# Kernel tuning notes

Hardware: AMD Instinct MI355X
Metric: run time of the kernel (lower is better)

## Reference

```python
import jax, jax.numpy as jnp
import numpy as np

B, N, W, H, D, HEADS, L, T, FT = 1, 8192, 32, 128, 128, 4, 3, 2048, 768
NW = N // W          # 256 query windows
DH = D // HEADS      # 32 head dim
NEG = jnp.float32(-1e9)

def _ln(x):
    m = jnp.mean(x, axis=-1, keepdims=True)
    v = jnp.var(x, axis=-1, keepdims=True)
    return (x - m) * jax.lax.rsqrt(v + 1e-5)

def setup_inputs():
    ks = iter(jax.random.split(jax.random.key(0), 40))
    f = lambda shape, s=0.02: jax.random.normal(next(ks), shape, jnp.float32) * s
    return dict(
        q=f((B, N, D), 1.0),
        c=f((B, N, D), 1.0),
        r=f((B, N, 3), 1.0),
        atom_enc_bias=f((B, NW, HEADS, W, H), 1.0),
        token_ids=jax.random.randint(next(ks), (B, N), 0, T),
        key_indices=jnp.sort(jax.random.randint(next(ks), (B, NW, H), 0, N), axis=-1),
        atom_pad_mask=jnp.ones((B, N), jnp.bool_),
        r_to_q_w=f((3, D)),
        adaln1_scale_w=f((L, D, D)), adaln1_shift_w=f((L, D, D)),
        wq=f((L, D, D)), bq=jnp.zeros((L, D), jnp.float32),
        wk=f((L, D, D)), wv=f((L, D, D)), wg=f((L, D, D)), wo=f((L, D, D)),
        wop=f((L, D, D)), bop=jnp.full((L, D), -2.0, jnp.float32),
        adaln2_scale_w=f((L, D, D)), adaln2_shift_w=f((L, D, D)),
        w_gate=f((L, D, 2 * D)), w_lin=f((L, D, 2 * D)), w2=f((L, 2 * D, D)),
        wg2=f((L, D, D)),
        w_a2t=f((D, FT)),
    )

def _forward(q, c, r, atom_enc_bias, r_to_q_w, adaln1_scale_w, adaln1_shift_w,
             wq, bq, wk, wv, wg, wo, wop, bop, adaln2_scale_w, adaln2_shift_w,
             w_gate, w_lin, w2, wg2, w_a2t, token_ids, key_indices, atom_pad_mask):
    a = q + r @ r_to_q_w                  # r_to_q_trans(r) added to q
    c_n = _ln(c)                          # AdaLN conditioning norm (shared)
    km = jnp.take_along_axis(atom_pad_mask, key_indices.reshape(B, NW * H), axis=1)
    km = km.reshape(B, NW, 1, 1, H)       # key mask for windowed attention
    inv_sqrt_dh = jnp.float32(1.0 / np.sqrt(DH))
    for l in range(L):
        # AdaLN + windowed attention with pair bias (DiffusionTransformer layer)
        b = jax.nn.sigmoid(c_n @ adaln1_scale_w[l]) * _ln(a) + c_n @ adaln1_shift_w[l]
        g = jax.nn.sigmoid(b @ wg[l]).reshape(B, NW, W, HEADS, DH)
        qh = (b @ wq[l] + bq[l]).reshape(B, NW, W, HEADS, DH)
        kv = jnp.take_along_axis(b, key_indices.reshape(B, NW * H, 1), axis=1)
        kv = kv.reshape(B, NW, H, D)      # to_keys(b): gather key atoms per window
        kh = (kv @ wk[l]).reshape(B, NW, H, HEADS, DH)
        vh = (kv @ wv[l]).reshape(B, NW, H, HEADS, DH)
        logits = jnp.einsum('bwqhd,bwkhd->bwhqk', qh, kh) * inv_sqrt_dh + atom_enc_bias
        logits = jnp.where(km, logits, NEG)
        attn = jax.nn.softmax(logits, axis=-1)
        o = jnp.einsum('bwhqk,bwkhd->bwqhd', attn, vh)
        o = ((g * o).reshape(B, N, D)) @ wo[l]
        a = a + jax.nn.sigmoid(c @ wop[l] + bop[l]) * o
        # conditioned transition block (SwiGLU, expansion 2)
        b = jax.nn.sigmoid(c_n @ adaln2_scale_w[l]) * _ln(a) + c_n @ adaln2_shift_w[l]
        h = jax.nn.silu(b @ w_gate[l]) * (b @ w_lin[l])
        a = a + jax.nn.sigmoid(c @ wg2[l]) * (h @ w2[l])
    # atom -> token mean pooling via dense one-hot bmm (the target op)
    q_to_a = jax.nn.relu(a @ w_a2t)                        # (B, N, FT)
    a2t = jax.nn.one_hot(token_ids, T, dtype=jnp.float32)  # (B, N, T) one-hot
    a2t_mean = a2t / (jnp.sum(a2t, axis=1, keepdims=True) + 1e-6)
    return jnp.einsum('bnt,bnf->btf', a2t_mean, q_to_a)    # (B, T, FT)

def reference(q, c, r, atom_enc_bias, token_ids, key_indices, atom_pad_mask,
              r_to_q_w, adaln1_scale_w, adaln1_shift_w, wq, bq, wk, wv, wg, wo,
              wop, bop, adaln2_scale_w, adaln2_shift_w, w_gate, w_lin, w2, wg2,
              w_a2t):
    return _forward(q, c, r, atom_enc_bias, r_to_q_w, adaln1_scale_w,
                    adaln1_shift_w, wq, bq, wk, wv, wg, wo, wop, bop,
                    adaln2_scale_w, adaln2_shift_w, w_gate, w_lin, w2, wg2,
                    w_a2t, token_ids, key_indices, atom_pad_mask)
```

## Files before the change

### kernel.cpp

```cpp
#include <hip/hip_runtime.h>
#include <cmath>

#define NA 8192
#define DM 128
#define NW_ 256
#define WQ 32
#define HK 128
#define NH 4
#define DH 32
#define NL 3
#define TT 2048
#define FT_ 768
#define DD ((size_t)DM * DM)
#define NM ((size_t)NA * DM)

typedef unsigned short u16;
typedef float f32x4 __attribute__((ext_vector_type(4)));
typedef short bhalf8 __attribute__((ext_vector_type(8)));

__device__ __forceinline__ float sigf(float x) { return 1.0f / (1.0f + expf(-x)); }

__device__ __forceinline__ u16 f2b(float f) {
    unsigned u = __builtin_bit_cast(unsigned, f);
    return (u16)((u + 0x7fffu + ((u >> 16) & 1u)) >> 16);
}
__device__ __forceinline__ float b2f(u16 u) {
    return __builtin_bit_cast(float, (unsigned)u << 16);
}
__device__ __forceinline__ void unpk2(unsigned u, float& lo, float& hi) {
    lo = __builtin_bit_cast(float, u << 16);
    hi = __builtin_bit_cast(float, u & 0xffff0000u);
}

__global__ __launch_bounds__(256) void convert_weights(
    const float* __restrict__ s1w, const float* __restrict__ sh1w,
    const float* __restrict__ s2w, const float* __restrict__ sh2w,
    const float* __restrict__ wop, const float* __restrict__ wg2,
    const float* __restrict__ wq, const float* __restrict__ wk,
    const float* __restrict__ wv, const float* __restrict__ wg,
    const float* __restrict__ wo, const float* __restrict__ wgate,
    const float* __restrict__ wlin, const float* __restrict__ w2,
    const float* __restrict__ wa2t, u16* __restrict__ wt)
{
    const int z = blockIdx.x;
    const float* src; int K, N; size_t off;
    if (z < 33) {
        K = 128; N = 128; off = (size_t)z * DD;
        const int fam = z / 3, l = z - fam * 3;
        switch (fam) {
            case 0: src = s1w; break;  case 1: src = sh1w; break;
            case 2: src = s2w; break;  case 3: src = sh2w; break;
            case 4: src = wop; break;  case 5: src = wg2; break;
            case 6: src = wq; break;   case 7: src = wk; break;
            case 8: src = wv; break;   case 9: src = wg; break;
            default: src = wo; break;
        }
        src += (size_t)l * DD;
    } else if (z < 39) {
        K = 128; N = 256; off = 33 * DD + (size_t)(z - 33) * 2 * DD;
        src = (z < 36) ? wgate + (size_t)(z - 33) * 2 * DD
                       : wlin + (size_t)(z - 36) * 2 * DD;
    } else if (z < 42) {
        K = 256; N = 128; off = 45 * DD + (size_t)(z - 39) * 2 * DD;
        src = w2 + (size_t)(z - 39) * 2 * DD;
    } else {
        K = 128; N = 768; off = 51 * DD; src = wa2t;
    }
    const int kb = (K == 256) ? 8 : 7;
    const int nchunk = N >> 3;
    const int n0 = blockIdx.y * nchunk;
    u16* dst = wt + off;
    for (int f = threadIdx.x; f < (nchunk << kb); f += 256) {
        const int nl = f >> kb, k = f & (K - 1);
        dst[(size_t)(n0 + nl) * K + k] = f2b(src[(size_t)k * N + n0 + nl]);
    }
}

__device__ __forceinline__ void stage_tile(const u16* __restrict__ src, int row0,
                                           int ld, int k0, u16* dst)
{
#pragma unroll
    for (int i = 0; i < 4; ++i) {
        const int flat = (i << 8) + threadIdx.x;
        const int r = flat >> 4, s = flat & 15;
        const uint4 v = *reinterpret_cast<const uint4*>(
            src + (size_t)(row0 + r) * ld + k0 + (((s ^ (r & 7)) << 3)));
        *reinterpret_cast<uint4*>(dst + r * 128 + (s << 3)) = v;
    }
}

__device__ __forceinline__ void stage_ln(const float* __restrict__ a,
                                         const u16* __restrict__ sp,
                                         const u16* __restrict__ sh,
                                         int row0, u16* dst)
{
#pragma unroll
    for (int i = 0; i < 4; ++i) {
        const int flat = (i << 8) + threadIdx.x;
        const int r = flat >> 4, s = flat & 15;
        const int cs = s ^ (r & 7);
        const float* srcp = a + (size_t)(row0 + r) * 128 + (cs << 3);
        const float4 v0 = *reinterpret_cast<const float4*>(srcp);
        const float4 v1 = *reinterpret_cast<const float4*>(srcp + 4);
        float vv[8] = {v0.x, v0.y, v0.z, v0.w, v1.x, v1.y, v1.z, v1.w};
        float sum = 0.f, sq = 0.f;
#pragma unroll
        for (int e = 0; e < 8; ++e) { sum += vv[e]; sq += vv[e] * vv[e]; }
#pragma unroll
        for (int off = 8; off >= 1; off >>= 1) {
            sum += __shfl_xor(sum, off, 64);
            sq  += __shfl_xor(sq, off, 64);
        }
        const float m = sum * (1.0f / 128.0f);
        const float inv = rsqrtf(sq * (1.0f / 128.0f) - m * m + 1e-5f);
        const uint4 spv = *reinterpret_cast<const uint4*>(
            sp + (size_t)(row0 + r) * 128 + (cs << 3));
        const uint4 shv = *reinterpret_cast<const uint4*>(
            sh + (size_t)(row0 + r) * 128 + (cs << 3));
        float spf[8], shf[8];
        unpk2(spv.x, spf[0], spf[1]); unpk2(spv.y, spf[2], spf[3]);
        unpk2(spv.z, spf[4], spf[5]); unpk2(spv.w, spf[6], spf[7]);
        unpk2(shv.x, shf[0], shf[1]); unpk2(shv.y, shf[2], shf[3]);
        unpk2(shv.z, shf[4], shf[5]); unpk2(shv.w, shf[6], shf[7]);
        u16 outv[8];
#pragma unroll
        for (int e = 0; e < 8; ++e)
            outv[e] = f2b(spf[e] * (vv[e] - m) * inv + shf[e]);
        *reinterpret_cast<uint4*>(dst + r * 128 + (s << 3)) =
            *reinterpret_cast<uint4*>(outv);
    }
}

__device__ __forceinline__ f32x4 mfma_bf16(bhalf8 a, bhalf8 b, f32x4 c) {
    return __builtin_amdgcn_mfma_f32_16x16x32_bf16(a, b, c, 0, 0, 0);
}

__device__ __forceinline__ void mfma_tile128(const u16* As, const u16* Bs,
                                             int wm, int wn, int lr, int lk,
                                             f32x4 (&acc)[2][2])
{
#pragma unroll
    for (int kt = 0; kt < 4; ++kt) {
        const int j = (kt << 2) + lk;
        bhalf8 af[2], bf[2];
#pragma unroll
        for (int mf = 0; mf < 2; ++mf) {
            const int R = wm * 32 + mf * 16 + lr;
            af[mf] = *reinterpret_cast<const bhalf8*>(&As[R * 128 + ((j ^ (R & 7)) << 3)]);
        }
#pragma unroll
        for (int nf = 0; nf < 2; ++nf) {
            const int C = wn * 32 + nf * 16 + lr;
            bf[nf] = *reinterpret_cast<const bhalf8*>(&Bs[C * 128 + ((j ^ (C & 7)) << 3)]);
        }
#pragma unroll
        for (int mf = 0; mf < 2; ++mf)
#pragma unroll
            for (int nf = 0; nf < 2; ++nf)
                acc[mf][nf] = mfma_bf16(af[mf], bf[nf], acc[mf][nf]);
    }
}

template <int KTOT>
__device__ __forceinline__ void mcore(const u16* __restrict__ A,
                                      const u16* __restrict__ Wt,
                                      int m0, int n0, u16* As, u16* Bs,
                                      int wm, int wn, int lr, int lk,
                                      f32x4 (&acc)[2][2])
{
#pragma unroll
    for (int k0 = 0; k0 < KTOT; k0 += 128) {
        if (k0) __syncthreads();
        stage_tile(A, m0, KTOT, k0, As);
        stage_tile(Wt, n0, KTOT, k0, Bs);
        __syncthreads();
        mfma_tile128(As, Bs, wm, wn, lr, lk, acc);
    }
}

#define EPI_SETUP                                                         \
    const int lane = threadIdx.x & 63, w = threadIdx.x >> 6;              \
    const int wm = w >> 1, wn = w & 1, lr = lane & 15, lk = lane >> 4;    \
    const int m0 = blockIdx.x << 6, n0 = blockIdx.y << 6;
#define EPI_ROW (m0 + wm * 32 + mf * 16 + (lk << 2) + r)
#define EPI_COL (n0 + wn * 32 + nf * 16 + lr)

__global__ __launch_bounds__(256) void precompute_m(const u16* __restrict__ cnb,
                                                    const u16* __restrict__ cb,
                                                    const u16* __restrict__ wt,
                                                    const float* __restrict__ bop,
                                                    u16* __restrict__ pre)
{
    __shared__ u16 As[64 * 128], Bs[64 * 128];
    const int z = blockIdx.z;
    const u16* A = (z < 12) ? cnb : cb;
    const u16* Wt = wt + (size_t)z * DD;
    const bool sig = (z < 3) || (z >= 6 && z < 9) || (z >= 12);
    const float* bias = (z >= 12 && z < 15) ? bop + (size_t)(z - 12) * DM : nullptr;
    EPI_SETUP
    f32x4 acc[2][2] = {};
    mcore<128>(A, Wt, m0, n0, As, Bs, wm, wn, lr, lk, acc);
    u16* out = pre + (size_t)z * NM;
#pragma unroll
    for (int mf = 0; mf < 2; ++mf)
#pragma unroll
        for (int nf = 0; nf < 2; ++nf)
#pragma unroll
            for (int r = 0; r < 4; ++r) {
                float v = acc[mf][nf][r];
                const int col = EPI_COL;
                if (bias) v += bias[col];
                if (sig) v = sigf(v);
                out[(size_t)EPI_ROW * DM + col] = f2b(v);
            }
}

__global__ __launch_bounds__(256) void qgkv_m(const float* __restrict__ a,
                                              const u16* __restrict__ sp,
                                              const u16* __restrict__ sh,
                                              const u16* __restrict__ wt, int l,
                                              const float* __restrict__ bq,
                                              u16* __restrict__ qh, u16* __restrict__ gb,
                                              u16* __restrict__ kf, u16* __restrict__ vf)
{
    __shared__ u16 As[64 * 128], Bs[64 * 128];
    const int z = blockIdx.z;
    const int wi = (z == 0 ? 18 : z == 1 ? 27 : z == 2 ? 21 : 24) + l;
    EPI_SETUP
    f32x4 acc[2][2] = {};
    stage_ln(a, sp, sh, m0, As);
    stage_tile(wt + (size_t)wi * DD, n0, 128, 0, Bs);
    __syncthreads();
    mfma_tile128(As, Bs, wm, wn, lr, lk, acc);
#pragma unroll
    for (int mf = 0; mf < 2; ++mf)
#pragma unroll
        for (int nf = 0; nf < 2; ++nf)
#pragma unroll
            for (int r = 0; r < 4; ++r) {
                const int col = EPI_COL;
                const size_t off = (size_t)EPI_ROW * DM + col;
                const float v = acc[mf][nf][r];
                if (z == 0)      qh[off] = f2b(v + bq[col]);
                else if (z == 1) gb[off] = f2b(sigf(v));
                else if (z == 2) kf[off] = f2b(v);
                else             vf[off] = f2b(v);
            }
}

__global__ __launch_bounds__(256) void attn_m(const u16* __restrict__ qh,
                                              const u16* __restrict__ kf,
                                              const u16* __restrict__ vf,
                                              const int* __restrict__ kidx,
                                              const float* __restrict__ bias,
                                              const u16* __restrict__ gb,
                                              u16* __restrict__ ob)
{
    __shared__ __align__(16) unsigned char smem[47616];
    int*   idx_s = (int*)smem;
    u16*   Qs = (u16*)(smem + 512);
    u16*   Ks = (u16*)(smem + 3072);
    u16*   Vt = (u16*)(smem + 13312);
    u16*   Ps = (u16*)(smem + 22016);
    float* Ls = (float*)(smem + 30720);

    const int wdw = blockIdx.x, h = blockIdx.y;
    const int tid = threadIdx.x;
    const int lane = tid & 63, w = tid >> 6;
    const int lr = lane & 15, lk = lane >> 4;

    if (tid < 128) {
        idx_s[tid] = kidx[wdw * HK + tid];
        const int qi = tid >> 2, cs = (tid & 3) << 3;
        const uint4 v = *reinterpret_cast<const uint4*>(
            qh + (size_t)(wdw * WQ + qi) * DM + h * DH + cs);
        *reinterpret_cast<uint4*>(&Qs[qi * 40 + cs]) = v;
    }
    __syncthreads();
#pragma unroll
    for (int i = 0; i < 2; ++i) {
        const int flat = (i << 8) + tid;
        const int kr = flat >> 2, cs = (flat & 3) << 3;
        const size_t src = (size_t)idx_s[kr] * DM + h * DH + cs;
        const uint4 kv = *reinterpret_cast<const uint4*>(kf + src);
        *reinterpret_cast<uint4*>(&Ks[kr * 40 + cs]) = kv;
        const uint4 vv = *reinterpret_cast<const uint4*>(vf + src);
        const u16* ve = reinterpret_cast<const u16*>(&vv);
#pragma unroll
        for (int e = 0; e < 8; ++e) Vt[(cs + e) * 136 + kr] = ve[e];
    }
    __syncthreads();

    {
        const float scale = 0.17677669529663687f;
        bhalf8 af[2];
        af[0] = *reinterpret_cast<const bhalf8*>(&Qs[lr * 40 + lk * 8]);
        af[1] = *reinterpret_cast<const bhalf8*>(&Qs[(16 + lr) * 40 + lk * 8]);
        f32x4 acc[2][2];
#pragma unroll
        for (int nf = 0; nf < 2; ++nf) {
            const int key = w * 32 + nf * 16 + lr;
            const bhalf8 bf = *reinterpret_cast<const bhalf8*>(&Ks[key * 40 + lk * 8]);
            f32x4 z = {0.f, 0.f, 0.f, 0.f};
            acc[0][nf] = mfma_bf16(af[0], bf, z);
            acc[1][nf] = mfma_bf16(af[1], bf, z);
        }
        const float* bb = bias + ((size_t)(wdw * NH + h) * WQ) * HK;
#pragma unroll
        for (int mf = 0; mf < 2; ++mf)
#pragma unroll
            for (int nf = 0; nf < 2; ++nf)
#pragma unroll
                for (int r = 0; r < 4; ++r) {
                    const int row = mf * 16 + (lk << 2) + r;
                    const int col = w * 32 + nf * 16 + lr;
                    Ls[row * 132 + col] = acc[mf][nf][r] * scale + bb[row * HK + col];
                }
    }
    __syncthreads();

    {
        const int row = tid >> 3, sub = tid & 7;
        float x[16];
#pragma unroll
        for (int i = 0; i < 16; ++i) x[i] = Ls[row * 132 + sub * 16 + i];
        float mx = x[0];
#pragma unroll
        for (int i = 1; i < 16; ++i) mx = fmaxf(mx, x[i]);
#pragma unroll
        for (int off = 4; off >= 1; off >>= 1) mx = fmaxf(mx, __shfl_xor(mx, off, 64));
        float s = 0.f;
#pragma unroll
        for (int i = 0; i < 16; ++i) { x[i] = expf(x[i] - mx); s += x[i]; }
#pragma unroll
        for (int off = 4; off >= 1; off >>= 1) s += __shfl_xor(s, off, 64);
        const float inv = 1.0f / s;
        u16 pv[16];
#pragma unroll
        for (int i = 0; i < 16; ++i) pv[i] = f2b(x[i] * inv);
        *reinterpret_cast<uint4*>(&Ps[row * 136 + sub * 16]) =
            *reinterpret_cast<uint4*>(pv);
        *reinterpret_cast<uint4*>(&Ps[row * 136 + sub * 16 + 8]) =
            *reinterpret_cast<uint4*>(pv + 8);
    }
    __syncthreads();

    {
        const int mf = w >> 1, nf = w & 1;
        f32x4 acc = {0.f, 0.f, 0.f, 0.f};
#pragma unroll
        for (int ks = 0; ks < 4; ++ks) {
            const bhalf8 af = *reinterpret_cast<const bhalf8*>(
                &Ps[(mf * 16 + lr) * 136 + ks * 32 + lk * 8]);
            const bhalf8 bf = *reinterpret_cast<const bhalf8*>(
                &Vt[(nf * 16 + lr) * 136 + ks * 32 + lk * 8]);
            acc = mfma_bf16(af, bf, acc);
        }
#pragma unroll
        for (int r = 0; r < 4; ++r) {
            const int row = wdw * WQ + mf * 16 + (lk << 2) + r;
            const int col = h * DH + nf * 16 + lr;
            const size_t off = (size_t)row * DM + col;
            ob[off] = f2b(b2f(gb[off]) * acc[r]);
        }
    }
}

__global__ __launch_bounds__(256) void swiglu_m(const float* __restrict__ a,
                                                const u16* __restrict__ sp,
                                                const u16* __restrict__ sh,
                                                const u16* __restrict__ wga,
                                                const u16* __restrict__ wli,
                                                u16* __restrict__ h)
{
    __shared__ u16 As[64 * 128], B1[64 * 128], B2[64 * 128];
    EPI_SETUP
    f32x4 a1[2][2] = {}, a2[2][2] = {};
    stage_ln(a, sp, sh, m0, As);
    stage_tile(wga, n0, 128, 0, B1);
    stage_tile(wli, n0, 128, 0, B2);
    __syncthreads();
    mfma_tile128(As, B1, wm, wn, lr, lk, a1);
    mfma_tile128(As, B2, wm, wn, lr, lk, a2);
#pragma unroll
    for (int mf = 0; mf < 2; ++mf)
#pragma unroll
        for (int nf = 0; nf < 2; ++nf)
#pragma unroll
            for (int r = 0; r < 4; ++r) {
                const float x = a1[mf][nf][r];
                h[(size_t)EPI_ROW * 256 + EPI_COL] = f2b(x * sigf(x) * a2[mf][nf][r]);
            }
}

template <int KTOT>
__global__ __launch_bounds__(256) void res_m(const u16* __restrict__ Ab,
                                             const u16* __restrict__ Wt,
                                             const u16* __restrict__ gate,
                                             float* __restrict__ a,
                                             u16* __restrict__ abf)
{
    __shared__ u16 As[64 * 128], Bs[64 * 128];
    EPI_SETUP
    f32x4 acc[2][2] = {};
    mcore<KTOT>(Ab, Wt, m0, n0, As, Bs, wm, wn, lr, lk, acc);
#pragma unroll
    for (int mf = 0; mf < 2; ++mf)
#pragma unroll
        for (int nf = 0; nf < 2; ++nf)
#pragma unroll
            for (int r = 0; r < 4; ++r) {
                const size_t off = (size_t)EPI_ROW * DM + EPI_COL;
                const float v = a[off] + b2f(gate[off]) * acc[mf][nf][r];
                a[off] = v;
                abf[off] = f2b(v);
            }
}

__global__ __launch_bounds__(256) void a2t_m(const u16* __restrict__ Ab,
                                             const u16* __restrict__ Wt,
                                             const int* __restrict__ tokens,
                                             const int* __restrict__ counts,
                                             float* __restrict__ out)
{
    __shared__ u16 As[64 * 128], Bs[64 * 128];
    EPI_SETUP
    f32x4 acc[2][2] = {};
    mcore<128>(Ab, Wt, m0, n0, As, Bs, wm, wn, lr, lk, acc);
#pragma unroll
    for (int mf = 0; mf < 2; ++mf)
#pragma unroll
        for (int nf = 0; nf < 2; ++nf)
#pragma unroll
            for (int r = 0; r < 4; ++r) {
                const int row = EPI_ROW;
                const int tok = tokens[row];
                const float sc = 1.0f / ((float)counts[tok] + 1e-6f);
                atomicAdd(out + (size_t)tok * FT_ + EPI_COL,
                          fmaxf(acc[mf][nf][r], 0.f) * sc);
            }
}

__global__ __launch_bounds__(256) void ln_init(const float* __restrict__ q,
                                               const float* __restrict__ r,
                                               const float* __restrict__ r2q,
                                               const float* __restrict__ c,
                                               float* __restrict__ a,
                                               u16* __restrict__ cnb,
                                               u16* __restrict__ cb)
{
    const int wave = threadIdx.x >> 6, lane = threadIdx.x & 63;
    const int row = (blockIdx.x << 2) + wave;
    const size_t base = (size_t)row * DM;
    const float r0 = r[row * 3 + 0], r1 = r[row * 3 + 1], r2 = r[row * 3 + 2];
    a[base + lane] = q[base + lane] + r0 * r2q[lane] + r1 * r2q[DM + lane]
                     + r2 * r2q[2 * DM + lane];
    a[base + lane + 64] = q[base + lane + 64] + r0 * r2q[lane + 64]
                          + r1 * r2q[DM + lane + 64] + r2 * r2q[2 * DM + lane + 64];
    float x0 = c[base + lane], x1 = c[base + lane + 64];
    cb[base + lane] = f2b(x0); cb[base + lane + 64] = f2b(x1);
    float s = x0 + x1, sq = x0 * x0 + x1 * x1;
#pragma unroll
    for (int off = 32; off >= 1; off >>= 1) {
        s += __shfl_xor(s, off, 64);
        sq += __shfl_xor(sq, off, 64);
    }
    const float m = s * (1.0f / 128.0f);
    const float var = sq * (1.0f / 128.0f) - m * m;
    const float inv = rsqrtf(var + 1e-5f);
    cnb[base + lane]      = f2b((x0 - m) * inv);
    cnb[base + lane + 64] = f2b((x1 - m) * inv);
}

__global__ __launch_bounds__(256) void count_tokens(const int* __restrict__ tok,
                                                    int* __restrict__ cnt)
{
    atomicAdd(&cnt[tok[blockIdx.x * 256 + threadIdx.x]], 1);
}

extern "C" void kernel_launch(void* const* d_in, const int* in_sizes, int n_in,
                              void* d_out, int out_size, void* d_ws, size_t ws_size,
                              hipStream_t stream)
{
    (void)in_sizes; (void)n_in; (void)ws_size;
    const float* q_in  = (const float*)d_in[0];
    const float* c_in  = (const float*)d_in[1];
    const float* r_in  = (const float*)d_in[2];
    const float* bias  = (const float*)d_in[3];
    const int*   tok   = (const int*)d_in[4];
    const int*   kidx  = (const int*)d_in[5];
    const float* r2q   = (const float*)d_in[7];
    const float* s1w   = (const float*)d_in[8];
    const float* sh1w  = (const float*)d_in[9];
    const float* wq    = (const float*)d_in[10];
    const float* bq    = (const float*)d_in[11];
    const float* wk    = (const float*)d_in[12];
    const float* wv    = (const float*)d_in[13];
    const float* wg    = (const float*)d_in[14];
    const float* wo    = (const float*)d_in[15];
    const float* wop   = (const float*)d_in[16];
    const float* bop   = (const float*)d_in[17];
    const float* s2w   = (const float*)d_in[18];
    const float* sh2w  = (const float*)d_in[19];
    const float* wgate = (const float*)d_in[20];
    const float* wlin  = (const float*)d_in[21];
    const float* w2    = (const float*)d_in[22];
    const float* wg2   = (const float*)d_in[23];
    const float* wa2t  = (const float*)d_in[24];
    float* out = (float*)d_out;

    float* ws = (float*)d_ws;
    float* a_ = ws;
    u16* u    = (u16*)(ws + NM);
    u16* pre_ = u;
    u16* qhb_ = u + 18 * NM;
    u16* gb_  = u + 19 * NM;
    u16* kfb_ = u + 20 * NM;
    u16* vfb_ = u + 21 * NM;
    u16* hb_  = u + 22 * NM;
    u16* abf_ = u + 24 * NM;
    u16* cnb_ = u + 25 * NM;
    u16* cb_  = u + 26 * NM;
    u16* wt_  = u + 27 * NM;
    u16* ob_  = u + 28 * NM;
    int* cnt_ = (int*)(u + 29 * NM);

    hipMemsetAsync(d_out, 0, sizeof(float) * (size_t)out_size, stream);
    hipMemsetAsync(cnt_, 0, sizeof(int) * TT, stream);

    convert_weights<<<dim3(43, 8), 256, 0, stream>>>(
        s1w, sh1w, s2w, sh2w, wop, wg2, wq, wk, wv, wg, wo, wgate, wlin, w2, wa2t, wt_);
    ln_init<<<NA / 4, 256, 0, stream>>>(q_in, r_in, r2q, c_in, a_, cnb_, cb_);
    count_tokens<<<NA / 256, 256, 0, stream>>>(tok, cnt_);
    precompute_m<<<dim3(128, 2, 18), 256, 0, stream>>>(cnb_, cb_, wt_, bop, pre_);

    for (int l = 0; l < NL; ++l) {
        const u16* S1p  = pre_ + (size_t)(0 + l) * NM;
        const u16* Sh1p = pre_ + (size_t)(3 + l) * NM;
        const u16* S2p  = pre_ + (size_t)(6 + l) * NM;
        const u16* Sh2p = pre_ + (size_t)(9 + l) * NM;
        const u16* Gop  = pre_ + (size_t)(12 + l) * NM;
        const u16* Gg2  = pre_ + (size_t)(15 + l) * NM;

        qgkv_m<<<dim3(128, 2, 4), 256, 0, stream>>>(
            a_, S1p, Sh1p, wt_, l, bq + (size_t)l * DM, qhb_, gb_, kfb_, vfb_);
        attn_m<<<dim3(NW_, NH), 256, 0, stream>>>(qhb_, kfb_, vfb_, kidx, bias, gb_, ob_);
        res_m<128><<<dim3(128, 2), 256, 0, stream>>>(
            ob_, wt_ + (size_t)(30 + l) * DD, Gop, a_, abf_);
        swiglu_m<<<dim3(128, 4), 256, 0, stream>>>(
            a_, S2p, Sh2p, wt_ + (33 + 2 * (size_t)l) * DD,
            wt_ + (39 + 2 * (size_t)l) * DD, hb_);
        res_m<256><<<dim3(128, 2), 256, 0, stream>>>(
            hb_, wt_ + (45 + 2 * (size_t)l) * DD, Gg2, a_, abf_);
    }

    a2t_m<<<dim3(128, 12), 256, 0, stream>>>(abf_, wt_ + 51 * DD, tok, cnt_, out);
}
```

Measured before the change: 313.4 us.

## Widen GEMM tiles to 64x128, merge prep kernels, fold attention scale into Q

Precompute, qgkv and a2t GEMMs now use 64x128 output tiles per block, with each wave computing 16 rows across 128 columns. This halves the block count and avoids re-staging the A tile once per 64-column slice. The separate weight-convert, LN-init and token-count kernels are merged into one prep launch to cut launch overhead. The 1/sqrt(dh) attention scale moves into the Q projection epilogue, so the attention kernel no longer multiplies the logits. The cost is double the shared memory per block, more accumulators per wave and fewer blocks, which may lower occupancy and parallelism.

```diff
diff --git a/kernel.cpp b/kernel.cpp
--- a/kernel.cpp
+++ b/kernel.cpp
@@ -32,7 +32,7 @@
     hi = __builtin_bit_cast(float, u & 0xffff0000u);
 }
 
-__global__ __launch_bounds__(256) void convert_weights(
+__global__ __launch_bounds__(256) void prep(
     const float* __restrict__ s1w, const float* __restrict__ sh1w,
     const float* __restrict__ s2w, const float* __restrict__ sh2w,
     const float* __restrict__ wop, const float* __restrict__ wg2,
@@ -40,39 +40,69 @@
     const float* __restrict__ wv, const float* __restrict__ wg,
     const float* __restrict__ wo, const float* __restrict__ wgate,
     const float* __restrict__ wlin, const float* __restrict__ w2,
-    const float* __restrict__ wa2t, u16* __restrict__ wt)
-{
-    const int z = blockIdx.x;
-    const float* src; int K, N; size_t off;
-    if (z < 33) {
-        K = 128; N = 128; off = (size_t)z * DD;
-        const int fam = z / 3, l = z - fam * 3;
-        switch (fam) {
-            case 0: src = s1w; break;  case 1: src = sh1w; break;
-            case 2: src = s2w; break;  case 3: src = sh2w; break;
-            case 4: src = wop; break;  case 5: src = wg2; break;
-            case 6: src = wq; break;   case 7: src = wk; break;
-            case 8: src = wv; break;   case 9: src = wg; break;
-            default: src = wo; break;
-        }
-        src += (size_t)l * DD;
-    } else if (z < 39) {
-        K = 128; N = 256; off = 33 * DD + (size_t)(z - 33) * 2 * DD;
-        src = (z < 36) ? wgate + (size_t)(z - 33) * 2 * DD
-                       : wlin + (size_t)(z - 36) * 2 * DD;
-    } else if (z < 42) {
-        K = 256; N = 128; off = 45 * DD + (size_t)(z - 39) * 2 * DD;
-        src = w2 + (size_t)(z - 39) * 2 * DD;
+    const float* __restrict__ wa2t, u16* __restrict__ wt,
+    const float* __restrict__ q_in, const float* __restrict__ r_in,
+    const float* __restrict__ r2q, const float* __restrict__ c_in,
+    float* __restrict__ a, u16* __restrict__ cnb, u16* __restrict__ cb,
+    const int* __restrict__ tok, int* __restrict__ cnt)
+{
+    const int bx = blockIdx.x;
+    if (bx < 344) {
+        const int z = bx >> 3;
+        const float* src; int K, N; size_t off;
+        if (z < 33) {
+            K = 128; N = 128; off = (size_t)z * DD;
+            const int fam = z / 3, l = z - fam * 3;
+            switch (fam) {
+                case 0: src = s1w; break;  case 1: src = sh1w; break;
+                case 2: src = s2w; break;  case 3: src = sh2w; break;
+                case 4: src = wop; break;  case 5: src = wg2; break;
+                case 6: src = wq; break;   case 7: src = wk; break;
+                case 8: src = wv; break;   case 9: src = wg; break;
+                default: src = wo; break;
+            }
+            src += (size_t)l * DD;
+        } else if (z < 39) {
+            K = 128; N = 256; off = 33 * DD + (size_t)(z - 33) * 2 * DD;
+            src = (z < 36) ? wgate + (size_t)(z - 33) * 2 * DD
+                           : wlin + (size_t)(z - 36) * 2 * DD;
+        } else if (z < 42) {
+            K = 256; N = 128; off = 45 * DD + (size_t)(z - 39) * 2 * DD;
+            src = w2 + (size_t)(z - 39) * 2 * DD;
+        } else {
+            K = 128; N = 768; off = 51 * DD; src = wa2t;
+        }
+        const int kb = (K == 256) ? 8 : 7;
+        const int nchunk = N >> 3;
+        const int n0 = (bx & 7) * nchunk;
+        u16* dst = wt + off;
+        for (int f = threadIdx.x; f < (nchunk << kb); f += 256) {
+            const int nl = f >> kb, k = f & (K - 1);
+            dst[(size_t)(n0 + nl) * K + k] = f2b(src[(size_t)k * N + n0 + nl]);
+        }
+    } else if (bx < 2392) {
+        const int wave = threadIdx.x >> 6, lane = threadIdx.x & 63;
+        const int row = ((bx - 344) << 2) + wave;
+        const size_t base = (size_t)row * DM;
+        const float r0 = r_in[row * 3 + 0], r1 = r_in[row * 3 + 1], r2 = r_in[row * 3 + 2];
+        a[base + lane] = q_in[base + lane] + r0 * r2q[lane] + r1 * r2q[DM + lane]
+                         + r2 * r2q[2 * DM + lane];
+        a[base + lane + 64] = q_in[base + lane + 64] + r0 * r2q[lane + 64]
+                              + r1 * r2q[DM + lane + 64] + r2 * r2q[2 * DM + lane + 64];
+        float x0 = c_in[base + lane], x1 = c_in[base + lane + 64];
+        cb[base + lane] = f2b(x0); cb[base + lane + 64] = f2b(x1);
+        float s = x0 + x1, sq = x0 * x0 + x1 * x1;
+#pragma unroll
+        for (int off = 32; off >= 1; off >>= 1) {
+            s += __shfl_xor(s, off, 64);
+            sq += __shfl_xor(sq, off, 64);
+        }
+        const float m = s * (1.0f / 128.0f);
+        const float inv = rsqrtf(sq * (1.0f / 128.0f) - m * m + 1e-5f);
+        cnb[base + lane]      = f2b((x0 - m) * inv);
+        cnb[base + lane + 64] = f2b((x1 - m) * inv);
     } else {
-        K = 128; N = 768; off = 51 * DD; src = wa2t;
-    }
-    const int kb = (K == 256) ? 8 : 7;
-    const int nchunk = N >> 3;
-    const int n0 = blockIdx.y * nchunk;
-    u16* dst = wt + off;
-    for (int f = threadIdx.x; f < (nchunk << kb); f += 256) {
-        const int nl = f >> kb, k = f & (K - 1);
-        dst[(size_t)(n0 + nl) * K + k] = f2b(src[(size_t)k * N + n0 + nl]);
+        atomicAdd(&cnt[tok[(bx - 2392) * 256 + threadIdx.x]], 1);
     }
 }
 
@@ -81,6 +111,19 @@
 {
 #pragma unroll
     for (int i = 0; i < 4; ++i) {
+        const int flat = (i << 8) + threadIdx.x;
+        const int r = flat >> 4, s = flat & 15;
+        const uint4 v = *reinterpret_cast<const uint4*>(
+            src + (size_t)(row0 + r) * ld + k0 + (((s ^ (r & 7)) << 3)));
+        *reinterpret_cast<uint4*>(dst + r * 128 + (s << 3)) = v;
+    }
+}
+
+__device__ __forceinline__ void stage_tile128(const u16* __restrict__ src, int row0,
+                                              int ld, int k0, u16* dst)
+{
+#pragma unroll
+    for (int i = 0; i < 8; ++i) {
         const int flat = (i << 8) + threadIdx.x;
         const int r = flat >> 4, s = flat & 15;
         const uint4 v = *reinterpret_cast<const uint4*>(
@@ -178,12 +221,34 @@
     }
 }
 
+__device__ __forceinline__ void mfma_wide(const u16* As, const u16* Bs,
+                                          int w, int lr, int lk, f32x4 (&acc)[8])
+{
+#pragma unroll
+    for (int kt = 0; kt < 4; ++kt) {
+        const int j = (kt << 2) + lk;
+        const int R = w * 16 + lr;
+        const bhalf8 af = *reinterpret_cast<const bhalf8*>(&As[R * 128 + ((j ^ (R & 7)) << 3)]);
+#pragma unroll
+        for (int nf = 0; nf < 8; ++nf) {
+            const int C = nf * 16 + lr;
+            const bhalf8 bf = *reinterpret_cast<const bhalf8*>(&Bs[C * 128 + ((j ^ (C & 7)) << 3)]);
+            acc[nf] = mfma_bf16(af, bf, acc[nf]);
+        }
+    }
+}
+
 #define EPI_SETUP                                                         \
     const int lane = threadIdx.x & 63, w = threadIdx.x >> 6;              \
     const int wm = w >> 1, wn = w & 1, lr = lane & 15, lk = lane >> 4;    \
     const int m0 = blockIdx.x << 6, n0 = blockIdx.y << 6;
 #define EPI_ROW (m0 + wm * 32 + mf * 16 + (lk << 2) + r)
 #define EPI_COL (n0 + wn * 32 + nf * 16 + lr)
+#define WEPI_SETUP                                                        \
+    const int lane = threadIdx.x & 63, w = threadIdx.x >> 6;              \
+    const int lr = lane & 15, lk = lane >> 4;                             \
+    const int m0 = blockIdx.x << 6;
+#define WEPI_ROW (m0 + w * 16 + (lk << 2) + r)
 
 __global__ __launch_bounds__(256) void precompute_m(const u16* __restrict__ cnb,
                                                     const u16* __restrict__ cb,
@@ -191,28 +256,29 @@
                                                     const float* __restrict__ bop,
                                                     u16* __restrict__ pre)
 {
-    __shared__ u16 As[64 * 128], Bs[64 * 128];
-    const int z = blockIdx.z;
+    __shared__ u16 As[64 * 128], Bs[128 * 128];
+    const int z = blockIdx.y;
     const u16* A = (z < 12) ? cnb : cb;
     const u16* Wt = wt + (size_t)z * DD;
     const bool sig = (z < 3) || (z >= 6 && z < 9) || (z >= 12);
     const float* bias = (z >= 12 && z < 15) ? bop + (size_t)(z - 12) * DM : nullptr;
-    EPI_SETUP
-    f32x4 acc[2][2] = {};
-    mcore<128>(A, Wt, m0, n0, As, Bs, wm, wn, lr, lk, acc);
+    WEPI_SETUP
+    f32x4 acc[8] = {};
+    stage_tile(A, m0, 128, 0, As);
+    stage_tile128(Wt, 0, 128, 0, Bs);
+    __syncthreads();
+    mfma_wide(As, Bs, w, lr, lk, acc);
     u16* out = pre + (size_t)z * NM;
 #pragma unroll
-    for (int mf = 0; mf < 2; ++mf)
-#pragma unroll
-        for (int nf = 0; nf < 2; ++nf)
-#pragma unroll
-            for (int r = 0; r < 4; ++r) {
-                float v = acc[mf][nf][r];
-                const int col = EPI_COL;
-                if (bias) v += bias[col];
-                if (sig) v = sigf(v);
-                out[(size_t)EPI_ROW * DM + col] = f2b(v);
-            }
+    for (int nf = 0; nf < 8; ++nf)
+#pragma unroll
+        for (int r = 0; r < 4; ++r) {
+            float v = acc[nf][r];
+            const int col = nf * 16 + lr;
+            if (bias) v += bias[col];
+            if (sig) v = sigf(v);
+            out[(size_t)WEPI_ROW * DM + col] = f2b(v);
+        }
 }
 
 __global__ __launch_bounds__(256) void qgkv_m(const float* __restrict__ a,
@@ -223,29 +289,28 @@
                                               u16* __restrict__ qh, u16* __restrict__ gb,
                                               u16* __restrict__ kf, u16* __restrict__ vf)
 {
-    __shared__ u16 As[64 * 128], Bs[64 * 128];
-    const int z = blockIdx.z;
+    __shared__ u16 As[64 * 128], Bs[128 * 128];
+    const int z = blockIdx.y;
     const int wi = (z == 0 ? 18 : z == 1 ? 27 : z == 2 ? 21 : 24) + l;
-    EPI_SETUP
-    f32x4 acc[2][2] = {};
+    WEPI_SETUP
+    f32x4 acc[8] = {};
     stage_ln(a, sp, sh, m0, As);
-    stage_tile(wt + (size_t)wi * DD, n0, 128, 0, Bs);
-    __syncthreads();
-    mfma_tile128(As, Bs, wm, wn, lr, lk, acc);
-#pragma unroll
-    for (int mf = 0; mf < 2; ++mf)
-#pragma unroll
-        for (int nf = 0; nf < 2; ++nf)
-#pragma unroll
-            for (int r = 0; r < 4; ++r) {
-                const int col = EPI_COL;
-                const size_t off = (size_t)EPI_ROW * DM + col;
-                const float v = acc[mf][nf][r];
-                if (z == 0)      qh[off] = f2b(v + bq[col]);
-                else if (z == 1) gb[off] = f2b(sigf(v));
-                else if (z == 2) kf[off] = f2b(v);
-                else             vf[off] = f2b(v);
-            }
+    stage_tile128(wt + (size_t)wi * DD, 0, 128, 0, Bs);
+    __syncthreads();
+    mfma_wide(As, Bs, w, lr, lk, acc);
+    const float qscale = 0.17677669529663687f;
+#pragma unroll
+    for (int nf = 0; nf < 8; ++nf)
+#pragma unroll
+        for (int r = 0; r < 4; ++r) {
+            const int col = nf * 16 + lr;
+            const size_t off = (size_t)WEPI_ROW * DM + col;
+            const float v = acc[nf][r];
+            if (z == 0)      qh[off] = f2b((v + bq[col]) * qscale);
+            else if (z == 1) gb[off] = f2b(sigf(v));
+            else if (z == 2) kf[off] = f2b(v);
+            else             vf[off] = f2b(v);
+        }
 }
 
 __global__ __launch_bounds__(256) void attn_m(const u16* __restrict__ qh,
@@ -292,7 +357,6 @@
     __syncthreads();
 
     {
-        const float scale = 0.17677669529663687f;
         bhalf8 af[2];
         af[0] = *reinterpret_cast<const bhalf8*>(&Qs[lr * 40 + lk * 8]);
         af[1] = *reinterpret_cast<const bhalf8*>(&Qs[(16 + lr) * 40 + lk * 8]);
@@ -314,7 +378,7 @@
                 for (int r = 0; r < 4; ++r) {
                     const int row = mf * 16 + (lk << 2) + r;
                     const int col = w * 32 + nf * 16 + lr;
-                    Ls[row * 132 + col] = acc[mf][nf][r] * scale + bb[row * HK + col];
+                    Ls[row * 132 + col] = acc[mf][nf][r] + bb[row * HK + col];
                 }
     }
     __syncthreads();
@@ -423,59 +487,24 @@
                                              const int* __restrict__ counts,
                                              float* __restrict__ out)
 {
-    __shared__ u16 As[64 * 128], Bs[64 * 128];
-    EPI_SETUP
-    f32x4 acc[2][2] = {};
-    mcore<128>(Ab, Wt, m0, n0, As, Bs, wm, wn, lr, lk, acc);
-#pragma unroll
-    for (int mf = 0; mf < 2; ++mf)
-#pragma unroll
-        for (int nf = 0; nf < 2; ++nf)
-#pragma unroll
-            for (int r = 0; r < 4; ++r) {
-                const int row = EPI_ROW;
-                const int tok = tokens[row];
-                const float sc = 1.0f / ((float)counts[tok] + 1e-6f);
-                atomicAdd(out + (size_t)tok * FT_ + EPI_COL,
-                          fmaxf(acc[mf][nf][r], 0.f) * sc);
-            }
-}
-
-__global__ __launch_bounds__(256) void ln_init(const float* __restrict__ q,
-                                               const float* __restrict__ r,
-                                               const float* __restrict__ r2q,
-                                               const float* __restrict__ c,
-                                               float* __restrict__ a,
-                                               u16* __restrict__ cnb,
-                                               u16* __restrict__ cb)
-{
-    const int wave = threadIdx.x >> 6, lane = threadIdx.x & 63;
-    const int row = (blockIdx.x << 2) + wave;
-    const size_t base = (size_t)row * DM;
-    const float r0 = r[row * 3 + 0], r1 = r[row * 3 + 1], r2 = r[row * 3 + 2];
-    a[base + lane] = q[base + lane] + r0 * r2q[lane] + r1 * r2q[DM + lane]
-                     + r2 * r2q[2 * DM + lane];
-    a[base + lane + 64] = q[base + lane + 64] + r0 * r2q[lane + 64]
-                          + r1 * r2q[DM + lane + 64] + r2 * r2q[2 * DM + lane + 64];
-    float x0 = c[base + lane], x1 = c[base + lane + 64];
-    cb[base + lane] = f2b(x0); cb[base + lane + 64] = f2b(x1);
-    float s = x0 + x1, sq = x0 * x0 + x1 * x1;
-#pragma unroll
-    for (int off = 32; off >= 1; off >>= 1) {
-        s += __shfl_xor(s, off, 64);
-        sq += __shfl_xor(sq, off, 64);
-    }
-    const float m = s * (1.0f / 128.0f);
-    const float var = sq * (1.0f / 128.0f) - m * m;
-    const float inv = rsqrtf(var + 1e-5f);
-    cnb[base + lane]      = f2b((x0 - m) * inv);
-    cnb[base + lane + 64] = f2b((x1 - m) * inv);
-}
-
-__global__ __launch_bounds__(256) void count_tokens(const int* __restrict__ tok,
-                                                    int* __restrict__ cnt)
-{
-    atomicAdd(&cnt[tok[blockIdx.x * 256 + threadIdx.x]], 1);
+    __shared__ u16 As[64 * 128], Bs[128 * 128];
+    WEPI_SETUP
+    const int n0 = blockIdx.y << 7;
+    f32x4 acc[8] = {};
+    stage_tile(Ab, m0, 128, 0, As);
+    stage_tile128(Wt, n0, 128, 0, Bs);
+    __syncthreads();
+    mfma_wide(As, Bs, w, lr, lk, acc);
+#pragma unroll
+    for (int nf = 0; nf < 8; ++nf)
+#pragma unroll
+        for (int r = 0; r < 4; ++r) {
+            const int row = WEPI_ROW;
+            const int tok = tokens[row];
+            const float sc = 1.0f / ((float)counts[tok] + 1e-6f);
+            atomicAdd(out + (size_t)tok * FT_ + n0 + nf * 16 + lr,
+                      fmaxf(acc[nf][r], 0.f) * sc);
+        }
 }
 
 extern "C" void kernel_launch(void* const* d_in, const int* in_sizes, int n_in,
@@ -528,11 +557,10 @@
     hipMemsetAsync(d_out, 0, sizeof(float) * (size_t)out_size, stream);
     hipMemsetAsync(cnt_, 0, sizeof(int) * TT, stream);
 
-    convert_weights<<<dim3(43, 8), 256, 0, stream>>>(
-        s1w, sh1w, s2w, sh2w, wop, wg2, wq, wk, wv, wg, wo, wgate, wlin, w2, wa2t, wt_);
-    ln_init<<<NA / 4, 256, 0, stream>>>(q_in, r_in, r2q, c_in, a_, cnb_, cb_);
-    count_tokens<<<NA / 256, 256, 0, stream>>>(tok, cnt_);
-    precompute_m<<<dim3(128, 2, 18), 256, 0, stream>>>(cnb_, cb_, wt_, bop, pre_);
+    prep<<<2424, 256, 0, stream>>>(
+        s1w, sh1w, s2w, sh2w, wop, wg2, wq, wk, wv, wg, wo, wgate, wlin, w2, wa2t, wt_,
+        q_in, r_in, r2q, c_in, a_, cnb_, cb_, tok, cnt_);
+    precompute_m<<<dim3(128, 18), 256, 0, stream>>>(cnb_, cb_, wt_, bop, pre_);
 
     for (int l = 0; l < NL; ++l) {
         const u16* S1p  = pre_ + (size_t)(0 + l) * NM;
@@ -542,7 +570,7 @@
         const u16* Gop  = pre_ + (size_t)(12 + l) * NM;
         const u16* Gg2  = pre_ + (size_t)(15 + l) * NM;
 
-        qgkv_m<<<dim3(128, 2, 4), 256, 0, stream>>>(
+        qgkv_m<<<dim3(128, 4), 256, 0, stream>>>(
             a_, S1p, Sh1p, wt_, l, bq + (size_t)l * DM, qhb_, gb_, kfb_, vfb_);
         attn_m<<<dim3(NW_, NH), 256, 0, stream>>>(qhb_, kfb_, vfb_, kidx, bias, gb_, ob_);
         res_m<128><<<dim3(128, 2), 256, 0, stream>>>(
@@ -554,5 +582,5 @@
             hb_, wt_ + (45 + 2 * (size_t)l) * DD, Gg2, a_, abf_);
     }
 
-    a2t_m<<<dim3(128, 12), 256, 0, stream>>>(abf_, wt_ + 51 * DD, tok, cnt_, out);
-}
+    a2t_m<<<dim3(128, 6), 256, 0, stream>>>(abf_, wt_ + 51 * DD, tok, cnt_, out);
+}
```

After: 318.7 us. About the same (+1.7%).
